# Performance work log

Measured on AMD Instinct MI355X. Metric: run time of the kernel, lower is better.

## Reference

```python
import jax, jax.numpy as jnp
import numpy as np

N, E = 10000, 320000
IN_CH, HID, OUT_CH, HEADS = 128, 64, 40, 8
NEG_SLOPE = 0.2


def gat_conv(x, src, dst, W, a_src, a_dst, bias, heads, C, concat, n_nodes):
    # x: [N, F_in]; W: [F_in, heads*C]; a_src/a_dst: [heads, C]
    h = (x @ W).reshape(n_nodes, heads, C)              # [N,H,C]
    alpha_src = jnp.sum(h * a_src, axis=-1)             # [N,H]
    alpha_dst = jnp.sum(h * a_dst, axis=-1)             # [N,H]
    score = jax.nn.leaky_relu(alpha_src[src] + alpha_dst[dst], NEG_SLOPE)  # [E,H]
    # segment softmax over edges sharing the same destination node
    smax = jax.ops.segment_max(score, dst, num_segments=n_nodes)
    smax = jnp.where(jnp.isfinite(smax), smax, 0.0)
    ex = jnp.exp(score - smax[dst])
    denom = jax.ops.segment_sum(ex, dst, num_segments=n_nodes)
    alpha = ex / (denom[dst] + 1e-16)                   # [E,H]
    msg = h[src] * alpha[:, :, None]                    # [E,H,C]
    out = jax.ops.segment_sum(msg, dst, num_segments=n_nodes)  # [N,H,C]
    out = out.reshape(n_nodes, heads * C) if concat else out.mean(axis=1)
    return out + bias


def setup_inputs() -> dict:
    key = jax.random.key(0)
    ks = jax.random.split(key, 16)
    g = 0.1
    return {
        "x": jax.random.normal(ks[0], (N, IN_CH), jnp.float32),
        "edge_index": jax.random.randint(ks[1], (2, E), 0, N, jnp.int64),
        "W1": jax.random.normal(ks[2], (IN_CH, HID), jnp.float32) * g,
        "b1": jnp.zeros((HID,), jnp.float32),
        "Wc1": jax.random.normal(ks[3], (HID, HEADS * HID), jnp.float32) * g,
        "att_src1": jax.random.normal(ks[4], (HEADS, HID), jnp.float32) * g,
        "att_dst1": jax.random.normal(ks[5], (HEADS, HID), jnp.float32) * g,
        "bc1": jnp.zeros((HEADS * HID,), jnp.float32),
        "Wc2": jax.random.normal(ks[6], (HEADS * HID, HID), jnp.float32) * g,
        "att_src2": jax.random.normal(ks[7], (1, HID), jnp.float32) * g,
        "att_dst2": jax.random.normal(ks[8], (1, HID), jnp.float32) * g,
        "bc2": jnp.zeros((HID,), jnp.float32),
        "W2": jax.random.normal(ks[9], (HID, OUT_CH), jnp.float32) * g,
        "b2": jnp.zeros((OUT_CH,), jnp.float32),
    }


def reference(x, edge_index, W1, b1, Wc1, att_src1, att_dst1, bc1,
              Wc2, att_src2, att_dst2, bc2, W2, b2):
    # add self-loops (PyG GATConv default add_self_loops=True)
    loop = jnp.arange(N, dtype=edge_index.dtype)
    src = jnp.concatenate([edge_index[0], loop])
    dst = jnp.concatenate([edge_index[1], loop])

    h = jax.nn.relu(x @ W1 + b1)                                   # lin0 + relu (dropout off in eval)
    h = jax.nn.elu(gat_conv(h, src, dst, Wc1, att_src1, att_dst1, bc1,
                            HEADS, HID, True, N))                  # conv1, concat heads
    h = gat_conv(h, src, dst, Wc2, att_src2, att_dst2, bc2,
                 1, HID, False, N)                                 # conv2, single head
    return h @ W2 + b2
```

## Files before the change

kernel.cpp:

```cpp
#include <hip/hip_runtime.h>
#include <cstdint>
#include <cstddef>

#define IN_CH 128
#define HID 64
#define HEADS 8
#define OUT_CH 40
#define NEG 0.2f
#define PAD 128

typedef __attribute__((ext_vector_type(8))) short bf16x8;
typedef __attribute__((ext_vector_type(4))) float f32x4;

#define MFMA(a, b, c) __builtin_amdgcn_mfma_f32_16x16x32_bf16(a, b, c, 0, 0, 0)

__device__ inline unsigned short f2bf(float f) {
    unsigned u = __float_as_uint(f);
    unsigned r = (u + 0x7FFFu + ((u >> 16) & 1u)) >> 16;
    return (unsigned short)r;
}
__device__ inline float bf2f(unsigned short b) {
    return __uint_as_float((unsigned)b << 16);
}
__device__ inline bf16x8 ldb8(const unsigned short* p) {
    return *reinterpret_cast<const bf16x8*>(p);
}


__global__ void k_init(const float* __restrict__ W1,
                       const float* __restrict__ Wc1, const float* __restrict__ Wc2,
                       const float* __restrict__ as1, const float* __restrict__ ad1,
                       int* __restrict__ cursor,
                       unsigned short* __restrict__ W1T,
                       unsigned short* __restrict__ Wc1T, unsigned short* __restrict__ Wc2T,
                       unsigned short* __restrict__ vaT, int N) {
    int i = blockIdx.x * 256 + threadIdx.x;
    if (i < N) { cursor[i] = 0; return; }
    i -= N;
    if (i < 64 * 128) {
        int j = i >> 7, k = i & 127;
        W1T[i] = f2bf(W1[k * 64 + j]);
        return;
    }
    i -= 64 * 128;
    if (i < 512 * 64) {
        int j = i >> 6, k = i & 63;
        Wc1T[i] = f2bf(Wc1[(size_t)k * 512 + j]);
        return;
    }
    i -= 512 * 64;
    if (i < 64 * 512) {
        int j = i >> 9, k = i & 511;
        Wc2T[i] = f2bf(Wc2[(size_t)k * 64 + j]);
        return;
    }
    i -= 64 * 512;
    if (i < 8192) {
        int u = i >> 3, q = i & 7;
        int t = u >> 6, k = u & 63;
        int h = t & 7;
        const float* a = (t < 8) ? as1 : ad1;
        float sum = 0.f;
#pragma unroll
        for (int c2 = q * 8; c2 < q * 8 + 8; ++c2)
            sum += Wc1[(size_t)k * 512 + h * 64 + c2] * a[h * 64 + c2];
        sum += __shfl_xor(sum, 1);
        sum += __shfl_xor(sum, 2);
        sum += __shfl_xor(sum, 4);
        if (q == 0) vaT[t * 64 + k] = f2bf(sum);
    }
}


__global__ __launch_bounds__(256) void k_lin1m(const float* __restrict__ x,
                                               const unsigned short* __restrict__ W1T,
                                               const float* __restrict__ b1,
                                               const unsigned short* __restrict__ vaT,
                                               unsigned short* __restrict__ h0b,
                                               float* __restrict__ asrc, float* __restrict__ adst,
                                               const int* __restrict__ ei, int E, int T,
                                               int* __restrict__ cursor, int* __restrict__ csrc,
                                               int N, int NB) {
    __shared__ unsigned short h0s[16][72];
    if (blockIdx.x >= NB) {
        int e = (blockIdx.x - NB) * 256 + threadIdx.x;
        if (e < T) {
            int s, d;
            if (e < E) { s = ei[e]; d = ei[E + e]; } else { s = d = e - E; }
            int pos = atomicAdd(&cursor[d], 1);
            csrc[(size_t)d * PAD + pos] = s;
        }
        return;
    }
    int w = threadIdx.x >> 6, l = threadIdx.x & 63;
    int m0 = blockIdx.x * 16;
    int c = l & 15, g = l >> 4;
    int xr = m0 + c; if (xr >= N) xr = N - 1;
    bf16x8 af[4];
    const float* arow = x + (size_t)xr * 128 + 8 * g;
#pragma unroll
    for (int ks = 0; ks < 4; ++ks) {
        float4 f0 = *(const float4*)(arow + 32 * ks);
        float4 f1 = *(const float4*)(arow + 32 * ks + 4);
        bf16x8 t;
        t[0] = (short)f2bf(f0.x); t[1] = (short)f2bf(f0.y);
        t[2] = (short)f2bf(f0.z); t[3] = (short)f2bf(f0.w);
        t[4] = (short)f2bf(f1.x); t[5] = (short)f2bf(f1.y);
        t[6] = (short)f2bf(f1.z); t[7] = (short)f2bf(f1.w);
        af[ks] = t;
    }
    const unsigned short* brow = W1T + (size_t)(16 * w + c) * 128 + 8 * g;
    f32x4 acca = {}, accb = {};
    acca = MFMA(af[0], ldb8(brow), acca);
    accb = MFMA(af[1], ldb8(brow + 32), accb);
    acca = MFMA(af[2], ldb8(brow + 64), acca);
    accb = MFMA(af[3], ldb8(brow + 96), accb);
    f32x4 acc = acca + accb;
    int j = 16 * w + c;
    float bj = b1[j];
#pragma unroll
    for (int r = 0; r < 4; ++r) {
        float v = fmaxf(acc[r] + bj, 0.f);
        unsigned short us = f2bf(v);
        int row = m0 + 4 * g + r;
        if (row < N) h0b[(size_t)row * 64 + j] = us;
        h0s[4 * g + r][j] = us;
    }
    __syncthreads();
    if (w == 0) {
        bf16x8 a0 = ldb8(&h0s[c][8 * g]);
        bf16x8 a1 = ldb8(&h0s[c][32 + 8 * g]);
        bf16x8 b0 = ldb8(&vaT[c * 64 + 8 * g]);
        bf16x8 b1v = ldb8(&vaT[c * 64 + 32 + 8 * g]);
        f32x4 al = {};
        al = MFMA(a0, b0, al);
        al = MFMA(a1, b1v, al);
#pragma unroll
        for (int r = 0; r < 4; ++r) {
            int n = m0 + 4 * g + r;
            if (n < N) {
                if (c < 8) asrc[n * 8 + c] = al[r];
                else       adst[n * 8 + (c - 8)] = al[r];
            }
        }
    }
}


__global__ __launch_bounds__(128) void k_conv1agg(const unsigned short* __restrict__ h0b,
                                                  const float* __restrict__ asrc, const float* __restrict__ adst,
                                                  const int* __restrict__ degs, const int* __restrict__ csrc,
                                                  unsigned short* __restrict__ aggb, int N) {
    __shared__ int srcb[PAD];
    __shared__ float sb[PAD][8];
    __shared__ float mx[8], den[8], adl[8];
    __shared__ float accsh[512];
    int tid = threadIdx.x;
    int n = blockIdx.x;
    int deg = degs[n];
    if (tid < 8) adl[tid] = adst[n * 8 + tid];
    __syncthreads();
    if (tid < deg) {
        int s = csrc[(size_t)n * PAD + tid];
        srcb[tid] = s;
        const float4* ap = (const float4*)&asrc[(size_t)s * 8];
        float4 a0 = ap[0], a1 = ap[1];
        float v;
        v = a0.x + adl[0]; sb[tid][0] = (v >= 0.f) ? v : NEG * v;
        v = a0.y + adl[1]; sb[tid][1] = (v >= 0.f) ? v : NEG * v;
        v = a0.z + adl[2]; sb[tid][2] = (v >= 0.f) ? v : NEG * v;
        v = a0.w + adl[3]; sb[tid][3] = (v >= 0.f) ? v : NEG * v;
        v = a1.x + adl[4]; sb[tid][4] = (v >= 0.f) ? v : NEG * v;
        v = a1.y + adl[5]; sb[tid][5] = (v >= 0.f) ? v : NEG * v;
        v = a1.z + adl[6]; sb[tid][6] = (v >= 0.f) ? v : NEG * v;
        v = a1.w + adl[7]; sb[tid][7] = (v >= 0.f) ? v : NEG * v;
    }
    __syncthreads();
    if (tid < 64) {
        int hh = tid & 7, idx = tid >> 3;
        float m = -1e30f;
        for (int i = idx; i < deg; i += 8) m = fmaxf(m, sb[i][hh]);
        m = fmaxf(m, __shfl_xor(m, 8));
        m = fmaxf(m, __shfl_xor(m, 16));
        m = fmaxf(m, __shfl_xor(m, 32));
        if (tid < 8) mx[tid] = m;
    }
    __syncthreads();
    if (tid < 64) {
        int hh = tid & 7, idx = tid >> 3;
        float mh = mx[hh];
        float d = 0.f;
        for (int i = idx; i < deg; i += 8) {
            float e = __expf(sb[i][hh] - mh);
            sb[i][hh] = e;
            d += e;
        }
        d += __shfl_xor(d, 8);
        d += __shfl_xor(d, 16);
        d += __shfl_xor(d, 32);
        if (tid < 8) den[tid] = d + 1e-16f;
    }
    __syncthreads();
    int lane = tid & 63, wv = tid >> 6;
    int half = lane >> 5, cl = lane & 31;
    float accA[8] = {0.f, 0.f, 0.f, 0.f, 0.f, 0.f, 0.f, 0.f};
    float accB[8] = {0.f, 0.f, 0.f, 0.f, 0.f, 0.f, 0.f, 0.f};
    for (int i = 2 * wv; i < deg; i += 4) {
        int e = i + half;
        float vx = 0.f, vy = 0.f;
        float4 w0 = {0.f, 0.f, 0.f, 0.f}, w1 = {0.f, 0.f, 0.f, 0.f};
        if (e < deg) {
            unsigned u = *(const unsigned*)&h0b[(size_t)srcb[e] * 64 + 2 * cl];
            vx = bf2f((unsigned short)(u & 0xFFFFu));
            vy = bf2f((unsigned short)(u >> 16));
            w0 = *(const float4*)&sb[e][0];
            w1 = *(const float4*)&sb[e][4];
        }
        accA[0] += w0.x * vx; accB[0] += w0.x * vy;
        accA[1] += w0.y * vx; accB[1] += w0.y * vy;
        accA[2] += w0.z * vx; accB[2] += w0.z * vy;
        accA[3] += w0.w * vx; accB[3] += w0.w * vy;
        accA[4] += w1.x * vx; accB[4] += w1.x * vy;
        accA[5] += w1.y * vx; accB[5] += w1.y * vy;
        accA[6] += w1.z * vx; accB[6] += w1.z * vy;
        accA[7] += w1.w * vx; accB[7] += w1.w * vy;
    }
#pragma unroll
    for (int h = 0; h < 8; ++h) {
        accA[h] += __shfl_xor(accA[h], 32);
        accB[h] += __shfl_xor(accB[h], 32);
    }
    __syncthreads();
    if (wv == 1 && half == 0) {
#pragma unroll
        for (int h = 0; h < 8; ++h) {
            accsh[h * 64 + 2 * cl] = accA[h];
            accsh[h * 64 + 2 * cl + 1] = accB[h];
        }
    }
    __syncthreads();
    if (wv == 0 && half == 0) {
#pragma unroll
        for (int h = 0; h < 8; ++h) {
            float t0 = (accA[h] + accsh[h * 64 + 2 * cl]) / den[h];
            float t1 = (accB[h] + accsh[h * 64 + 2 * cl + 1]) / den[h];
            unsigned uo = (unsigned)f2bf(t0) | ((unsigned)f2bf(t1) << 16);
            *(unsigned*)&aggb[(size_t)n * 512 + h * 64 + 2 * cl] = uo;
        }
    }
}


__global__ __launch_bounds__(256) void k_p1l2(const unsigned short* __restrict__ aggb,
                                              const unsigned short* __restrict__ Wc1T,
                                              const float* __restrict__ bc1,
                                              const unsigned short* __restrict__ Wc2T,
                                              const float* __restrict__ as2, const float* __restrict__ ad2,
                                              unsigned short* __restrict__ hc2b,
                                              float* __restrict__ asrc, float* __restrict__ adst, int N) {
    __shared__ unsigned short h1s[16][520];
    __shared__ float pps[4][16][2];
    int w = threadIdx.x >> 6, l = threadIdx.x & 63;
    int m0 = blockIdx.x * 16;
    int c = l & 15, g = l >> 4;
#pragma unroll
    for (int hl = 0; hl < 2; ++hl) {
        int h = 2 * w + hl;
        const unsigned short* arow = aggb + (size_t)(m0 + c) * 512 + h * 64 + 8 * g;
        bf16x8 af0 = ldb8(arow), af1 = ldb8(arow + 32);
        f32x4 acc[4] = {};
#pragma unroll
        for (int nt = 0; nt < 4; ++nt) {
            const unsigned short* brow = Wc1T + (size_t)(h * 64 + 16 * nt + c) * 64 + 8 * g;
            acc[nt] = MFMA(af0, ldb8(brow), acc[nt]);
            acc[nt] = MFMA(af1, ldb8(brow + 32), acc[nt]);
        }
#pragma unroll
        for (int nt = 0; nt < 4; ++nt) {
            int j = h * 64 + 16 * nt + c;
            float bj = bc1[j];
#pragma unroll
            for (int r = 0; r < 4; ++r) {
                float v = acc[nt][r] + bj;
                v = (v > 0.f) ? v : __expf(v) - 1.f;
                h1s[4 * g + r][j] = f2bf(v);
            }
        }
    }
    __syncthreads();
    const unsigned short* brow2 = Wc2T + (size_t)(16 * w + c) * 512 + 8 * g;
    f32x4 acc2a = {}, acc2b = {};
#pragma unroll
    for (int ks = 0; ks < 8; ++ks) {
        acc2a = MFMA(ldb8(&h1s[c][32 * ks + 8 * g]), ldb8(brow2 + 32 * ks), acc2a);
        acc2b = MFMA(ldb8(&h1s[c][32 * (ks + 8) + 8 * g]), ldb8(brow2 + 32 * (ks + 8)), acc2b);
    }
    f32x4 acc2 = acc2a + acc2b;
    int j = 16 * w + c;
    float aj = as2[j], dj = ad2[j];
    float ps[4], pd[4];
#pragma unroll
    for (int r = 0; r < 4; ++r) {
        float v = acc2[r];
        hc2b[(size_t)(m0 + 4 * g + r) * 64 + j] = f2bf(v);
        ps[r] = v * aj;
        pd[r] = v * dj;
    }
#pragma unroll
    for (int r = 0; r < 4; ++r) {
        float s = ps[r], d = pd[r];
        s += __shfl_xor(s, 1); s += __shfl_xor(s, 2); s += __shfl_xor(s, 4); s += __shfl_xor(s, 8);
        d += __shfl_xor(d, 1); d += __shfl_xor(d, 2); d += __shfl_xor(d, 4); d += __shfl_xor(d, 8);
        if (c == 0) {
            pps[w][4 * g + r][0] = s;
            pps[w][4 * g + r][1] = d;
        }
    }
    __syncthreads();
    int tid = threadIdx.x;
    if (tid < 32) {
        int row = tid >> 1, sel = tid & 1;
        float sum = pps[0][row][sel] + pps[1][row][sel] + pps[2][row][sel] + pps[3][row][sel];
        int n = m0 + row;
        if (n < N) {
            if (sel == 0) asrc[n] = sum;
            else          adst[n] = sum;
        }
    }
}


__global__ __launch_bounds__(256) void k_conv2f(const unsigned short* __restrict__ hc2b,
                                                const float* __restrict__ asrc, const float* __restrict__ adst,
                                                const int* __restrict__ degs, const int* __restrict__ csrc,
                                                const float* __restrict__ bc2,
                                                const float* __restrict__ W2, const float* __restrict__ b2,
                                                float* __restrict__ out, int N) {
    __shared__ float w2s[HID * OUT_CH];
    __shared__ float cosh_[4][HID];
    int tid = threadIdx.x;
    for (int i = tid; i < HID * OUT_CH; i += 256) w2s[i] = W2[i];
    int lane = tid & 63, nl = tid >> 6;
    int half = lane >> 5, cl = lane & 31;
    int n = blockIdx.x * 4 + nl;
    if (n < N) {
        int deg = degs[n];
        float ad = adst[n];
        float rm = -1e30f, rden = 0.f;
        float ax = 0.f, ay = 0.f;
        for (int base = 0; base < deg; base += 64) {
            int cnt = min(64, deg - base);
            int s = 0;
            float sc = -1e30f;
            if (lane < cnt) {
                s = csrc[(size_t)n * PAD + base + lane];
                float v = asrc[s] + ad;
                sc = (v >= 0.f) ? v : NEG * v;
            }
            float m = sc;
#pragma unroll
            for (int mm = 1; mm < 64; mm <<= 1) m = fmaxf(m, __shfl_xor(m, mm));
            float nmv = fmaxf(rm, m);
            float scale = __expf(rm - nmv);
            float p = (lane < cnt) ? __expf(sc - nmv) : 0.f;
            float d = p;
#pragma unroll
            for (int mm = 1; mm < 64; mm <<= 1) d += __shfl_xor(d, mm);
            rden = rden * scale + d;
            rm = nmv;
            ax *= scale; ay *= scale;
            for (int i = 0; i < cnt; i += 2) {
                int idx = i + half;
                float pi = __shfl(p, idx);
                int si = __shfl(s, idx);
                unsigned uu = *(const unsigned*)&hc2b[(size_t)si * 64 + 2 * cl];
                ax += pi * bf2f((unsigned short)(uu & 0xFFFFu));
                ay += pi * bf2f((unsigned short)(uu >> 16));
            }
        }
        ax += __shfl_xor(ax, 32);
        ay += __shfl_xor(ay, 32);
        if (half == 0) {
            float inv = 1.f / (rden + 1e-16f);
            cosh_[nl][2 * cl] = ax * inv + bc2[2 * cl];
            cosh_[nl][2 * cl + 1] = ay * inv + bc2[2 * cl + 1];
        }
    }
    __syncthreads();
    if (tid >= 160) return;
    int nn = tid / 40, j = tid % 40;
    int no = blockIdx.x * 4 + nn;
    if (no >= N) return;
    float s = b2[j];
#pragma unroll 8
    for (int k = 0; k < HID; ++k) s += cosh_[nn][k] * w2s[k * OUT_CH + j];
    out[(size_t)no * OUT_CH + j] = s;
}


extern "C" void kernel_launch(void* const* d_in, const int* in_sizes, int n_in,
                              void* d_out, int out_size, void* d_ws, size_t ws_size,
                              hipStream_t stream) {
    const float* x   = (const float*)d_in[0];
    const int*   ei  = (const int*)d_in[1];
    const float* W1  = (const float*)d_in[2];
    const float* b1  = (const float*)d_in[3];
    const float* Wc1 = (const float*)d_in[4];
    const float* as1 = (const float*)d_in[5];
    const float* ad1 = (const float*)d_in[6];
    const float* bc1 = (const float*)d_in[7];
    const float* Wc2 = (const float*)d_in[8];
    const float* as2 = (const float*)d_in[9];
    const float* ad2 = (const float*)d_in[10];
    const float* bc2 = (const float*)d_in[11];
    const float* W2  = (const float*)d_in[12];
    const float* b2  = (const float*)d_in[13];

    const int N = in_sizes[0] / IN_CH;
    const int E = in_sizes[1] / 2;
    const int T = E + N;

    char* base = (char*)d_ws;
    size_t off = 0;
    auto carve = [&](size_t bytes) -> void* {
        off = (off + 255) & ~(size_t)255;
        void* r = base + off;
        off += bytes;
        return r;
    };
    int* cursor     = (int*)carve((size_t)N * 4);
    int* csrc       = (int*)carve((size_t)N * PAD * 4);
    unsigned short* W1T  = (unsigned short*)carve((size_t)64 * 128 * 2);
    unsigned short* Wc1T = (unsigned short*)carve((size_t)512 * 64 * 2);
    unsigned short* Wc2T = (unsigned short*)carve((size_t)64 * 512 * 2);
    unsigned short* vaT  = (unsigned short*)carve((size_t)16 * 64 * 2);
    unsigned short* h0b  = (unsigned short*)carve((size_t)N * 64 * 2);
    float* asrc1    = (float*)carve((size_t)N * 8 * 4);
    float* adst1    = (float*)carve((size_t)N * 8 * 4);
    unsigned short* aggb = (unsigned short*)carve((size_t)N * 512 * 2);
    unsigned short* hc2b = (unsigned short*)carve((size_t)N * 64 * 2);
    float* asrc2    = (float*)carve((size_t)N * 4);
    float* adst2    = (float*)carve((size_t)N * 4);

    int init_total = N + 64 * 128 + 512 * 64 + 64 * 512 + 8192;
    k_init<<<(init_total + 255) / 256, 256, 0, stream>>>(W1, Wc1, Wc2, as1, ad1, cursor,
                                                         W1T, Wc1T, Wc2T, vaT, N);

    int NB = (N + 15) / 16;
    int FB = (T + 255) / 256;
    k_lin1m<<<NB + FB, 256, 0, stream>>>(x, W1T, b1, vaT, h0b, asrc1, adst1,
                                         ei, E, T, cursor, csrc, N, NB);
    k_conv1agg<<<N, 128, 0, stream>>>(h0b, asrc1, adst1, cursor, csrc, aggb, N);
    k_p1l2<<<(N + 15) / 16, 256, 0, stream>>>(aggb, Wc1T, bc1, Wc2T, as2, ad2,
                                              hc2b, asrc2, adst2, N);
    k_conv2f<<<(N + 3) / 4, 256, 0, stream>>>(hc2b, asrc2, adst2, cursor, csrc, bc2, W2, b2,
                                              (float*)d_out, N);
}
```

Measured before the change: 95.79 us.

## Compute conv1 neighbor aggregation with bf16 MFMA instead of scalar FMAs

The conv1 aggregation kernel now writes per-head softmax weights as bf16 into a 16xK LDS tile. It gathers neighbor features transposed into LDS and computes the weighted sum with 16x16x32 bf16 MFMA instructions, replacing the per-lane scalar FMA loop and the cross-wave shared-memory reduction. The score buffer aliases the new LDS tile to save space. The trade-off is an extra transposed LDS staging pass with possible bank conflicts, and attention weights rounded to bf16.

```diff
diff --git a/kernel.cpp b/kernel.cpp
--- a/kernel.cpp
+++ b/kernel.cpp
@@ -8,6 +8,7 @@
 #define OUT_CH 40
 #define NEG 0.2f
 #define PAD 128
+#define KP 136
 
 typedef __attribute__((ext_vector_type(8))) short bf16x8;
 typedef __attribute__((ext_vector_type(4))) float f32x4;
@@ -152,12 +153,14 @@
                                                   const int* __restrict__ degs, const int* __restrict__ csrc,
                                                   unsigned short* __restrict__ aggb, int N) {
     __shared__ int srcb[PAD];
-    __shared__ float sb[PAD][8];
     __shared__ float mx[8], den[8], adl[8];
-    __shared__ float accsh[512];
+    __shared__ unsigned short wA[16][KP];
+    __shared__ unsigned short BT[64][KP];
+    float (*sbf)[8] = (float(*)[8]) & BT[0][0];
     int tid = threadIdx.x;
     int n = blockIdx.x;
     int deg = degs[n];
+    int K32 = (deg + 31) & ~31;
     if (tid < 8) adl[tid] = adst[n * 8 + tid];
     __syncthreads();
     if (tid < deg) {
@@ -166,20 +169,23 @@
         const float4* ap = (const float4*)&asrc[(size_t)s * 8];
         float4 a0 = ap[0], a1 = ap[1];
         float v;
-        v = a0.x + adl[0]; sb[tid][0] = (v >= 0.f) ? v : NEG * v;
-        v = a0.y + adl[1]; sb[tid][1] = (v >= 0.f) ? v : NEG * v;
-        v = a0.z + adl[2]; sb[tid][2] = (v >= 0.f) ? v : NEG * v;
-        v = a0.w + adl[3]; sb[tid][3] = (v >= 0.f) ? v : NEG * v;
-        v = a1.x + adl[4]; sb[tid][4] = (v >= 0.f) ? v : NEG * v;
-        v = a1.y + adl[5]; sb[tid][5] = (v >= 0.f) ? v : NEG * v;
-        v = a1.z + adl[6]; sb[tid][6] = (v >= 0.f) ? v : NEG * v;
-        v = a1.w + adl[7]; sb[tid][7] = (v >= 0.f) ? v : NEG * v;
+        float4 s0, s1;
+        v = a0.x + adl[0]; s0.x = (v >= 0.f) ? v : NEG * v;
+        v = a0.y + adl[1]; s0.y = (v >= 0.f) ? v : NEG * v;
+        v = a0.z + adl[2]; s0.z = (v >= 0.f) ? v : NEG * v;
+        v = a0.w + adl[3]; s0.w = (v >= 0.f) ? v : NEG * v;
+        v = a1.x + adl[4]; s1.x = (v >= 0.f) ? v : NEG * v;
+        v = a1.y + adl[5]; s1.y = (v >= 0.f) ? v : NEG * v;
+        v = a1.z + adl[6]; s1.z = (v >= 0.f) ? v : NEG * v;
+        v = a1.w + adl[7]; s1.w = (v >= 0.f) ? v : NEG * v;
+        *(float4*)&sbf[tid][0] = s0;
+        *(float4*)&sbf[tid][4] = s1;
     }
     __syncthreads();
     if (tid < 64) {
         int hh = tid & 7, idx = tid >> 3;
         float m = -1e30f;
-        for (int i = idx; i < deg; i += 8) m = fmaxf(m, sb[i][hh]);
+        for (int i = idx; i < deg; i += 8) m = fmaxf(m, sbf[i][hh]);
         m = fmaxf(m, __shfl_xor(m, 8));
         m = fmaxf(m, __shfl_xor(m, 16));
         m = fmaxf(m, __shfl_xor(m, 32));
@@ -190,10 +196,10 @@
         int hh = tid & 7, idx = tid >> 3;
         float mh = mx[hh];
         float d = 0.f;
-        for (int i = idx; i < deg; i += 8) {
-            float e = __expf(sb[i][hh] - mh);
-            sb[i][hh] = e;
-            d += e;
+        for (int i = idx; i < K32; i += 8) {
+            float ev = 0.f;
+            if (i < deg) { ev = __expf(sbf[i][hh] - mh); d += ev; }
+            wA[hh][i] = f2bf(ev);
         }
         d += __shfl_xor(d, 8);
         d += __shfl_xor(d, 16);
@@ -201,51 +207,29 @@
         if (tid < 8) den[tid] = d + 1e-16f;
     }
     __syncthreads();
-    int lane = tid & 63, wv = tid >> 6;
-    int half = lane >> 5, cl = lane & 31;
-    float accA[8] = {0.f, 0.f, 0.f, 0.f, 0.f, 0.f, 0.f, 0.f};
-    float accB[8] = {0.f, 0.f, 0.f, 0.f, 0.f, 0.f, 0.f, 0.f};
-    for (int i = 2 * wv; i < deg; i += 4) {
-        int e = i + half;
-        float vx = 0.f, vy = 0.f;
-        float4 w0 = {0.f, 0.f, 0.f, 0.f}, w1 = {0.f, 0.f, 0.f, 0.f};
-        if (e < deg) {
-            unsigned u = *(const unsigned*)&h0b[(size_t)srcb[e] * 64 + 2 * cl];
-            vx = bf2f((unsigned short)(u & 0xFFFFu));
-            vy = bf2f((unsigned short)(u >> 16));
-            w0 = *(const float4*)&sb[e][0];
-            w1 = *(const float4*)&sb[e][4];
-        }
-        accA[0] += w0.x * vx; accB[0] += w0.x * vy;
-        accA[1] += w0.y * vx; accB[1] += w0.y * vy;
-        accA[2] += w0.z * vx; accB[2] += w0.z * vy;
-        accA[3] += w0.w * vx; accB[3] += w0.w * vy;
-        accA[4] += w1.x * vx; accB[4] += w1.x * vy;
-        accA[5] += w1.y * vx; accB[5] += w1.y * vy;
-        accA[6] += w1.z * vx; accB[6] += w1.z * vy;
-        accA[7] += w1.w * vx; accB[7] += w1.w * vy;
-    }
-#pragma unroll
-    for (int h = 0; h < 8; ++h) {
-        accA[h] += __shfl_xor(accA[h], 32);
-        accB[h] += __shfl_xor(accB[h], 32);
-    }
-    __syncthreads();
-    if (wv == 1 && half == 0) {
-#pragma unroll
-        for (int h = 0; h < 8; ++h) {
-            accsh[h * 64 + 2 * cl] = accA[h];
-            accsh[h * 64 + 2 * cl + 1] = accB[h];
-        }
-    }
-    __syncthreads();
-    if (wv == 0 && half == 0) {
-#pragma unroll
-        for (int h = 0; h < 8; ++h) {
-            float t0 = (accA[h] + accsh[h * 64 + 2 * cl]) / den[h];
-            float t1 = (accB[h] + accsh[h * 64 + 2 * cl + 1]) / den[h];
-            unsigned uo = (unsigned)f2bf(t0) | ((unsigned)f2bf(t1) << 16);
-            *(unsigned*)&aggb[(size_t)n * 512 + h * 64 + 2 * cl] = uo;
+    for (int idx = tid; idx < K32 * 32; idx += 128) {
+        int e = idx >> 5, cp = idx & 31;
+        unsigned u = 0;
+        if (e < deg) u = *(const unsigned*)&h0b[(size_t)srcb[e] * 64 + 2 * cp];
+        BT[2 * cp][e] = (unsigned short)(u & 0xFFFFu);
+        BT[2 * cp + 1][e] = (unsigned short)(u >> 16);
+    }
+    __syncthreads();
+    int w = tid >> 6, l = tid & 63;
+    int c = l & 15, g = l >> 4;
+    f32x4 acc0 = {}, acc1 = {};
+    for (int ks = 0; ks < (K32 >> 5); ++ks) {
+        bf16x8 af = ldb8(&wA[c][32 * ks + 8 * g]);
+        acc0 = MFMA(af, ldb8(&BT[32 * w + c][32 * ks + 8 * g]), acc0);
+        acc1 = MFMA(af, ldb8(&BT[32 * w + 16 + c][32 * ks + 8 * g]), acc1);
+    }
+    if (g < 2) {
+#pragma unroll
+        for (int r = 0; r < 4; ++r) {
+            int h = 4 * g + r;
+            float dh = den[h];
+            aggb[(size_t)n * 512 + h * 64 + 32 * w + c]      = f2bf(acc0[r] / dh);
+            aggb[(size_t)n * 512 + h * 64 + 32 * w + 16 + c] = f2bf(acc1[r] / dh);
         }
     }
 }
```

Result: slower. 111.5 us (+16.4%).
